# Optimization experiments

Hardware: AMD Instinct MI355X
Metric: run time of the kernel (lower is better)

The kernel has to match this reference:

```python
import jax, jax.numpy as jnp
import numpy as np

B, T, C = 2, 2048, 1024
H, D = 16, 64


def setup_inputs() -> dict:
    key = jax.random.key(0)
    k1, k2, k3 = jax.random.split(key, 3)
    x = jax.random.normal(k1, (B, T, C), dtype=jnp.float32)
    w_qkv = jax.random.normal(k2, (C, 3 * H * D), dtype=jnp.float32) * (C ** -0.5)
    w_proj = jax.random.normal(k3, (H * D, C), dtype=jnp.float32) * ((H * D) ** -0.5)
    sink_logit = jnp.zeros((H,), dtype=jnp.float32)
    return {"x": x, "w_qkv": w_qkv, "w_proj": w_proj, "sink_logit": sink_logit}


def reference(x, w_qkv, w_proj, sink_logit):
    b, t, c = x.shape
    qkv = x @ w_qkv                                  # [B,T,3HD]
    q, k, v = jnp.split(qkv, 3, axis=-1)
    # [B,H,T,D]
    q = q.reshape(b, t, H, D).transpose(0, 2, 1, 3)
    k = k.reshape(b, t, H, D).transpose(0, 2, 1, 3)
    v = v.reshape(b, t, H, D).transpose(0, 2, 1, 3)

    scale = 1.0 / jnp.sqrt(jnp.asarray(D, dtype=x.dtype))
    scores = jnp.einsum('bhqd,bhkd->bhqk', q, k) * scale   # [B,H,T,T]
    neg_inf = jnp.finfo(x.dtype).min
    causal = jnp.tril(jnp.ones((t, t), dtype=bool))
    scores = jnp.where(causal[None, None], scores, neg_inf)

    # sink column: per-head learnable logit b (added post-scale, V is zero)
    sink = jnp.broadcast_to(sink_logit.reshape(1, H, 1, 1), (b, H, t, 1)).astype(x.dtype)
    aug = jnp.concatenate([sink, scores], axis=-1)          # [B,H,T,T+1]
    attn = jax.nn.softmax(aug, axis=-1)
    # sink V is zero, so drop the sink column for the value contraction
    y = jnp.einsum('bhqk,bhkd->bhqd', attn[..., 1:], v)     # [B,H,T,D]
    y = y.transpose(0, 2, 1, 3).reshape(b, t, H * D)
    return y @ w_proj
```

## Files before the change

### kernel.cpp

```cpp
#include <hip/hip_runtime.h>
#include <hip/hip_bf16.h>
#include <stdint.h>

#define B_ 2
#define T_ 2048
#define C_ 1024
#define H_ 16
#define D_ 64

typedef __attribute__((ext_vector_type(8))) short short8;
typedef __attribute__((ext_vector_type(4))) float floatx4;

__device__ __forceinline__ float bf2f(uint16_t b) {
    return __uint_as_float(((uint32_t)b) << 16);
}
__device__ __forceinline__ uint16_t f2b(float f) {
    __hip_bfloat16 h = __float2bfloat16(f);
    return *(uint16_t*)&h;
}
__device__ __forceinline__ void glds16(const uint16_t* g, uint16_t* l) {
    __builtin_amdgcn_global_load_lds(
        (const __attribute__((address_space(1))) uint32_t*)g,
        (__attribute__((address_space(3))) uint32_t*)l, 16, 0, 0);
}

__global__ void canon_x(const float* __restrict__ in, uint16_t* __restrict__ out,
                        int n) {
    int i = (blockIdx.x * 256 + threadIdx.x) * 4;
    if (i >= n) return;
    float4 v = *(const float4*)(in + i);
    out[i + 0] = f2b(v.x);
    out[i + 1] = f2b(v.y);
    out[i + 2] = f2b(v.z);
    out[i + 3] = f2b(v.w);
}

__global__ void transpose_conv(const float* __restrict__ in, uint16_t* __restrict__ out,
                               int R, int W) {
    __shared__ uint16_t tile[32][33];
    int tx = threadIdx.x, ty = threadIdx.y;
    int c0 = blockIdx.x * 32, r0 = blockIdx.y * 32;
    #pragma unroll
    for (int i = 0; i < 32; i += 8)
        tile[ty + i][tx] = f2b(in[(size_t)(r0 + ty + i) * W + (c0 + tx)]);
    __syncthreads();
    #pragma unroll
    for (int i = 0; i < 32; i += 8)
        out[(size_t)(c0 + ty + i) * R + (r0 + tx)] = tile[tx][ty + i];
}

template <bool OUT_F32>
__global__ __launch_bounds__(256, 3)
void gemm_bt(const uint16_t* __restrict__ A, const uint16_t* __restrict__ Bt,
             void* __restrict__ Cv, int M, int N, int K) {
    __shared__ uint16_t As[3][128][32];
    __shared__ uint16_t Bs[3][128][32];
    int tid = threadIdx.x;
    int w = tid >> 6, lane = tid & 63;
    int quad = lane >> 4, l16 = lane & 15;
    int wr = (w >> 1) * 64, wc = (w & 1) * 64;

    int nwg = gridDim.x;
    int wg = (blockIdx.x & 7) * (nwg >> 3) + (blockIdx.x >> 3);
    int nby = N >> 7;
    int row0 = (wg / nby) * 128;
    int col0 = (wg % nby) * 128;

    int sr = w * 32 + (lane >> 2);
    int gsc = ((lane & 3) ^ ((lane >> 2) & 3)) * 8;
    uint16_t* lA0 = &As[0][sr][(lane & 3) * 8];
    uint16_t* lB0 = &Bs[0][sr][(lane & 3) * 8];
    const uint16_t* gA = A + (size_t)(row0 + sr) * K + gsc;
    const uint16_t* gB = Bt + (size_t)(col0 + sr) * K + gsc;

    floatx4 acc[4][4];
    #pragma unroll
    for (int i = 0; i < 4; i++)
        #pragma unroll
        for (int j = 0; j < 4; j++)
            acc[i][j] = (floatx4){0.f, 0.f, 0.f, 0.f};

#define STAGE3_(bs_, t_)                                                    \
    {                                                                       \
        const uint16_t* ga_ = gA + (size_t)(t_) * 32;                       \
        const uint16_t* gb_ = gB + (size_t)(t_) * 32;                       \
        uint16_t* la_ = lA0 + (bs_) * 4096;                                 \
        uint16_t* lb_ = lB0 + (bs_) * 4096;                                 \
        glds16(ga_, la_);                                                   \
        glds16(ga_ + 16 * K, la_ + 512);                                    \
        glds16(gb_, lb_);                                                   \
        glds16(gb_ + 16 * K, lb_ + 512);                                    \
    }

    int NT = K >> 5;
    STAGE3_(0, 0);
    STAGE3_(1, 1);
    asm volatile("s_waitcnt vmcnt(4)" ::: "memory");
    __builtin_amdgcn_s_barrier();

    const uint16_t* Ab = &As[0][0][0];
    const uint16_t* Bb = &Bs[0][0][0];
    int s = (quad ^ (l16 & 3)) * 8;
    int bc = 0, bs = 2;
    for (int t = 0; t < NT; ++t) {
        if (t + 2 < NT) STAGE3_(bs, t + 2);
        __builtin_amdgcn_sched_barrier(0);
        const uint16_t* Ac = Ab + bc * 4096;
        const uint16_t* Bc = Bb + bc * 4096;
        short8 af[4], bfr[4];
        #pragma unroll
        for (int i = 0; i < 4; i++)
            af[i] = *(const short8*)&Ac[(wr + i * 16 + l16) * 32 + s];
        #pragma unroll
        for (int j = 0; j < 4; j++)
            bfr[j] = *(const short8*)&Bc[(wc + j * 16 + l16) * 32 + s];
        #pragma unroll
        for (int i = 0; i < 4; i++)
            #pragma unroll
            for (int j = 0; j < 4; j++)
                acc[i][j] = __builtin_amdgcn_mfma_f32_16x16x32_bf16(
                    af[i], bfr[j], acc[i][j], 0, 0, 0);
        if (t + 2 < NT) {
            asm volatile("s_waitcnt vmcnt(4)" ::: "memory");
        } else {
            asm volatile("s_waitcnt vmcnt(0)" ::: "memory");
        }
        __builtin_amdgcn_s_barrier();
        bc = (bc == 2) ? 0 : bc + 1;
        bs = (bs == 2) ? 0 : bs + 1;
    }
#undef STAGE3_

    #pragma unroll
    for (int i = 0; i < 4; i++) {
        #pragma unroll
        for (int j = 0; j < 4; j++) {
            int rbase = row0 + wr + i * 16 + quad * 4;
            int cg = col0 + wc + j * 16 + l16;
            #pragma unroll
            for (int r = 0; r < 4; r++) {
                if (OUT_F32)
                    ((float*)Cv)[(size_t)(rbase + r) * N + cg] = acc[i][j][r];
                else
                    ((uint16_t*)Cv)[(size_t)(rbase + r) * N + cg] = f2b(acc[i][j][r]);
            }
        }
    }
}

__global__ __launch_bounds__(256, 2)
void attn_mfma(const uint16_t* __restrict__ qkv,
               const float* __restrict__ sink,
               uint16_t* __restrict__ y) {
    __shared__ uint16_t Ks[2][64][72];
    __shared__ uint16_t Vt[2][64][72];
    __shared__ uint16_t Pl[4][32][72];

    int tid = threadIdx.x;
    int w = tid >> 6, lane = tid & 63;
    int quad = lane >> 4, l16 = lane & 15;

    int id = blockIdx.x;
    int pair = id >> 5, bh = id & 31;
    int b = bh >> 4, h = bh & 15;
    int hi = 31 - pair, lo = pair;
    int q0s[2];
    q0s[0] = hi * 64 + w * 16;
    q0s[1] = lo * 64 + w * 16;
    int ktiles = hi + 1;
    int myk1 = lo + 1;

    const uint16_t* qkv_b = qkv + (size_t)b * T_ * 3072;

    short8 qf[2][2];
    #pragma unroll
    for (int qt = 0; qt < 2; qt++) {
        int qrow = q0s[qt] + l16;
        #pragma unroll
        for (int kd = 0; kd < 2; kd++) {
            uint4 raw = *(const uint4*)(qkv_b + (size_t)qrow * 3072 + h * 64 +
                                        kd * 32 + quad * 8);
            const uint16_t* rp = (const uint16_t*)&raw;
            short8 f;
            #pragma unroll
            for (int j = 0; j < 8; j++)
                f[j] = (short)f2b(bf2f(rp[j]) * 0.125f);
            qf[qt][kd] = f;
        }
    }

    float m_s[2], l_s[2];
    m_s[0] = m_s[1] = sink[h];
    l_s[0] = l_s[1] = 1.0f;
    floatx4 acc_o[2][4];
    #pragma unroll
    for (int qt = 0; qt < 2; qt++)
        #pragma unroll
        for (int dt = 0; dt < 4; dt++)
            acc_o[qt][dt] = (floatx4){0.f, 0.f, 0.f, 0.f};

    int t2 = tid >> 3;
    int dg = tid & 7;
    const uint16_t* kgp = qkv_b + 1024 + h * 64 + (size_t)(2 * t2) * 3072 + dg * 8;
    const uint16_t* vgp = kgp + 1024;
    int vcw = 2 * (t2 ^ (4 * dg));

    uint4 kr0 = *(const uint4*)(kgp);
    uint4 kr1 = *(const uint4*)(kgp + 3072);
    uint4 vr0 = *(const uint4*)(vgp);
    uint4 vr1 = *(const uint4*)(vgp + 3072);
    {
        *(uint4*)&Ks[0][2 * t2][dg * 8] = kr0;
        *(uint4*)&Ks[0][2 * t2 + 1][dg * 8] = kr1;
        const uint16_t* a0 = (const uint16_t*)&vr0;
        const uint16_t* a1 = (const uint16_t*)&vr1;
        #pragma unroll
        for (int j = 0; j < 8; j++)
            *(uint32_t*)&Vt[0][dg * 8 + j][vcw] =
                (uint32_t)a0[j] | ((uint32_t)a1[j] << 16);
    }
    if (ktiles > 1) {
        kr0 = *(const uint4*)(kgp + 64 * 3072);
        kr1 = *(const uint4*)(kgp + 64 * 3072 + 3072);
        vr0 = *(const uint4*)(vgp + 64 * 3072);
        vr1 = *(const uint4*)(vgp + 64 * 3072 + 3072);
    }
    __syncthreads();

    for (int kt = 0; kt < ktiles; kt++) {
        int cur = kt & 1;
        if (kt + 1 < ktiles) {
            *(uint4*)&Ks[cur ^ 1][2 * t2][dg * 8] = kr0;
            *(uint4*)&Ks[cur ^ 1][2 * t2 + 1][dg * 8] = kr1;
            const uint16_t* a0 = (const uint16_t*)&vr0;
            const uint16_t* a1 = (const uint16_t*)&vr1;
            #pragma unroll
            for (int j = 0; j < 8; j++)
                *(uint32_t*)&Vt[cur ^ 1][dg * 8 + j][vcw] =
                    (uint32_t)a0[j] | ((uint32_t)a1[j] << 16);
        }
        if (kt + 2 < ktiles) {
            size_t off = (size_t)(kt + 2) * 64 * 3072;
            kr0 = *(const uint4*)(kgp + off);
            kr1 = *(const uint4*)(kgp + off + 3072);
            vr0 = *(const uint4*)(vgp + off);
            vr1 = *(const uint4*)(vgp + off + 3072);
        }
        short8 kf[4][2];
        #pragma unroll
        for (int rt = 0; rt < 4; rt++) {
            kf[rt][0] = *(const short8*)&Ks[cur][rt * 16 + l16][quad * 8];
            kf[rt][1] = *(const short8*)&Ks[cur][rt * 16 + l16][32 + quad * 8];
        }
        short8 vf[2][4];
        #pragma unroll
        for (int kb = 0; kb < 2; kb++)
            #pragma unroll
            for (int dt = 0; dt < 4; dt++) {
                int d = dt * 16 + l16;
                int col = 2 * (((kb * 16) + quad * 4) ^ (4 * (d >> 3)));
                vf[kb][dt] = *(const short8*)&Vt[cur][d][col];
            }
        #pragma unroll
        for (int qt = 0; qt < 2; qt++) {
            if (qt == 1 && kt >= myk1) continue;
            floatx4 acc_s[4];
            #pragma unroll
            for (int rt = 0; rt < 4; rt++)
                acc_s[rt] = (floatx4){0.f, 0.f, 0.f, 0.f};
            #pragma unroll
            for (int rt = 0; rt < 4; rt++) {
                acc_s[rt] = __builtin_amdgcn_mfma_f32_16x16x32_bf16(
                    kf[rt][0], qf[qt][0], acc_s[rt], 0, 0, 0);
                acc_s[rt] = __builtin_amdgcn_mfma_f32_16x16x32_bf16(
                    kf[rt][1], qf[qt][1], acc_s[rt], 0, 0, 0);
            }
            int dqt = (qt == 0) ? hi : lo;
            if (kt == dqt) {
                int qg = q0s[qt] + l16;
                #pragma unroll
                for (int rt = 0; rt < 4; rt++) {
                    int kg = kt * 64 + rt * 16 + quad * 4;
                    #pragma unroll
                    for (int r = 0; r < 4; r++)
                        if (kg + r > qg) acc_s[rt][r] = -1e30f;
                }
            }
            float mx = -1e30f;
            #pragma unroll
            for (int rt = 0; rt < 4; rt++)
                #pragma unroll
                for (int r = 0; r < 4; r++) mx = fmaxf(mx, acc_s[rt][r]);
            mx = fmaxf(mx, __shfl_xor(mx, 16));
            mx = fmaxf(mx, __shfl_xor(mx, 32));
            float mnew = fmaxf(m_s[qt], mx);
            float alpha = __expf(m_s[qt] - mnew);
            m_s[qt] = mnew;
            float psum = 0.f;
            #pragma unroll
            for (int rt = 0; rt < 4; rt++) {
                float p0 = __expf(acc_s[rt][0] - mnew);
                float p1 = __expf(acc_s[rt][1] - mnew);
                float p2 = __expf(acc_s[rt][2] - mnew);
                float p3 = __expf(acc_s[rt][3] - mnew);
                psum += (p0 + p1) + (p2 + p3);
                uint2 pk;
                pk.x = (uint32_t)f2b(p0) | ((uint32_t)f2b(p1) << 16);
                pk.y = (uint32_t)f2b(p2) | ((uint32_t)f2b(p3) << 16);
                *(uint2*)&Pl[w][qt * 16 + l16][rt * 16 + quad * 4] = pk;
            }
            psum += __shfl_xor(psum, 16);
            psum += __shfl_xor(psum, 32);
            l_s[qt] = l_s[qt] * alpha + psum;
            #pragma unroll
            for (int r = 0; r < 4; r++) {
                float ar = __shfl(alpha, (lane & 48) | (quad * 4 + r));
                #pragma unroll
                for (int dt = 0; dt < 4; dt++) acc_o[qt][dt][r] *= ar;
            }
            #pragma unroll
            for (int kb = 0; kb < 2; kb++) {
                short8 pf = *(const short8*)&Pl[w][qt * 16 + l16][kb * 32 + quad * 8];
                #pragma unroll
                for (int dt = 0; dt < 4; dt++)
                    acc_o[qt][dt] = __builtin_amdgcn_mfma_f32_16x16x32_bf16(
                        pf, vf[kb][dt], acc_o[qt][dt], 0, 0, 0);
            }
        }
        __syncthreads();
    }

    #pragma unroll
    for (int qt = 0; qt < 2; qt++) {
        #pragma unroll
        for (int r = 0; r < 4; r++) {
            float lr = __shfl(l_s[qt], (lane & 48) | (quad * 4 + r));
            float inv = 1.0f / lr;
            int qg = q0s[qt] + quad * 4 + r;
            uint16_t* yp = y + (size_t)(b * T_ + qg) * 1024 + h * 64;
            #pragma unroll
            for (int dt = 0; dt < 4; dt++)
                yp[dt * 16 + l16] = f2b(acc_o[qt][dt][r] * inv);
        }
    }
}

extern "C" void kernel_launch(void* const* d_in, const int* in_sizes, int n_in,
                              void* d_out, int out_size, void* d_ws, size_t ws_size,
                              hipStream_t stream) {
    const float* x      = (const float*)d_in[0];
    const float* w_qkv  = (const float*)d_in[1];
    const float* w_proj = (const float*)d_in[2];
    const float* sink   = (const float*)d_in[3];
    float* out          = (float*)d_out;

    char* ws = (char*)d_ws;
    uint16_t* wt_qkv  = (uint16_t*)ws;
    uint16_t* wt_proj = (uint16_t*)(ws + 6291456);
    uint16_t* x_c     = (uint16_t*)(ws + 8388608);
    uint16_t* qkv     = (uint16_t*)(ws + 16777216);
    uint16_t* yb      = (uint16_t*)(ws + 41943040);

    canon_x<<<4194304 / 1024, 256, 0, stream>>>(x, x_c, 4194304);
    transpose_conv<<<dim3(3072 / 32, 1024 / 32), dim3(32, 8), 0, stream>>>(
        w_qkv, wt_qkv, 1024, 3072);
    transpose_conv<<<dim3(1024 / 32, 1024 / 32), dim3(32, 8), 0, stream>>>(
        w_proj, wt_proj, 1024, 1024);

    gemm_bt<false><<<dim3(768), 256, 0, stream>>>(
        x_c, wt_qkv, qkv, 4096, 3072, 1024);

    attn_mfma<<<dim3(16 * 32), 256, 0, stream>>>(qkv, sink, yb);

    gemm_bt<true><<<dim3(256), 256, 0, stream>>>(
        yb, wt_proj, out, 4096, 1024, 1024);
}
```

Baseline: 187.1 us.

## Fuse prep kernels, use exp2 softmax with lazy rescaling and packed bf16 convert

Merges the x-conversion and two weight-transpose kernels into a single prep launch to cut launch overhead. In attention, the log2(e) factor is folded into the Q scale and the sink logit so raw v_exp_f32 can replace __expf. The running max is only updated and the accumulators only rescaled when some lane's new max exceeds the old by more than 8, which skips the per-tile alpha shuffle and multiply in most iterations. P values are packed with v_cvt_pk_bf16_f32. The lazy threshold allows P values up to 2^8 before normalisation, which slightly changes numerics.

```diff
diff --git a/kernel.cpp b/kernel.cpp
--- a/kernel.cpp
+++ b/kernel.cpp
@@ -18,28 +18,51 @@
     __hip_bfloat16 h = __float2bfloat16(f);
     return *(uint16_t*)&h;
 }
+__device__ __forceinline__ float exp2v(float x) {
+    float r;
+    asm("v_exp_f32 %0, %1" : "=v"(r) : "v"(x));
+    return r;
+}
+__device__ __forceinline__ uint32_t cvtpk(float lo, float hi) {
+    uint32_t r;
+    asm("v_cvt_pk_bf16_f32 %0, %1, %2" : "=v"(r) : "v"(lo), "v"(hi));
+    return r;
+}
 __device__ __forceinline__ void glds16(const uint16_t* g, uint16_t* l) {
     __builtin_amdgcn_global_load_lds(
         (const __attribute__((address_space(1))) uint32_t*)g,
         (__attribute__((address_space(3))) uint32_t*)l, 16, 0, 0);
 }
 
-__global__ void canon_x(const float* __restrict__ in, uint16_t* __restrict__ out,
-                        int n) {
-    int i = (blockIdx.x * 256 + threadIdx.x) * 4;
-    if (i >= n) return;
-    float4 v = *(const float4*)(in + i);
-    out[i + 0] = f2b(v.x);
-    out[i + 1] = f2b(v.y);
-    out[i + 2] = f2b(v.z);
-    out[i + 3] = f2b(v.w);
-}
-
-__global__ void transpose_conv(const float* __restrict__ in, uint16_t* __restrict__ out,
-                               int R, int W) {
+__global__ void prep(const float* __restrict__ x, uint16_t* __restrict__ x_c,
+                     const float* __restrict__ w_qkv, uint16_t* __restrict__ wt_qkv,
+                     const float* __restrict__ w_proj, uint16_t* __restrict__ wt_proj) {
     __shared__ uint16_t tile[32][33];
-    int tx = threadIdx.x, ty = threadIdx.y;
-    int c0 = blockIdx.x * 32, r0 = blockIdx.y * 32;
+    int id = blockIdx.x;
+    int tid = threadIdx.x;
+    if (id < 4096) {
+        int i = (id * 256 + tid) * 4;
+        float4 v = *(const float4*)(x + i);
+        x_c[i + 0] = f2b(v.x);
+        x_c[i + 1] = f2b(v.y);
+        x_c[i + 2] = f2b(v.z);
+        x_c[i + 3] = f2b(v.w);
+        return;
+    }
+    const float* in;
+    uint16_t* out;
+    int R, W, bx, by;
+    if (id < 7168) {
+        int tb = id - 4096;
+        in = w_qkv; out = wt_qkv; R = 1024; W = 3072;
+        bx = tb % 96; by = tb / 96;
+    } else {
+        int tb = id - 7168;
+        in = w_proj; out = wt_proj; R = 1024; W = 1024;
+        bx = tb & 31; by = tb >> 5;
+    }
+    int tx = tid & 31, ty = tid >> 5;
+    int c0 = bx * 32, r0 = by * 32;
     #pragma unroll
     for (int i = 0; i < 32; i += 8)
         tile[ty + i][tx] = f2b(in[(size_t)(r0 + ty + i) * W + (c0 + tx)]);
@@ -172,6 +195,7 @@
 
     const uint16_t* qkv_b = qkv + (size_t)b * T_ * 3072;
 
+    const float QSC = 0.125f * 1.44269504f;
     short8 qf[2][2];
     #pragma unroll
     for (int qt = 0; qt < 2; qt++) {
@@ -184,13 +208,13 @@
             short8 f;
             #pragma unroll
             for (int j = 0; j < 8; j++)
-                f[j] = (short)f2b(bf2f(rp[j]) * 0.125f);
+                f[j] = (short)f2b(bf2f(rp[j]) * QSC);
             qf[qt][kd] = f;
         }
     }
 
     float m_s[2], l_s[2];
-    m_s[0] = m_s[1] = sink[h];
+    m_s[0] = m_s[1] = sink[h] * 1.44269504f;
     l_s[0] = l_s[1] = 1.0f;
     floatx4 acc_o[2][4];
     #pragma unroll
@@ -293,31 +317,36 @@
                 for (int r = 0; r < 4; r++) mx = fmaxf(mx, acc_s[rt][r]);
             mx = fmaxf(mx, __shfl_xor(mx, 16));
             mx = fmaxf(mx, __shfl_xor(mx, 32));
-            float mnew = fmaxf(m_s[qt], mx);
-            float alpha = __expf(m_s[qt] - mnew);
-            m_s[qt] = mnew;
+            float mold = m_s[qt];
+            if (!__all(mx <= mold + 8.0f)) {
+                float mnew = fmaxf(mold, mx);
+                float alpha = exp2v(mold - mnew);
+                m_s[qt] = mnew;
+                l_s[qt] *= alpha;
+                #pragma unroll
+                for (int r = 0; r < 4; r++) {
+                    float ar = __shfl(alpha, (lane & 48) | (quad * 4 + r));
+                    #pragma unroll
+                    for (int dt = 0; dt < 4; dt++) acc_o[qt][dt][r] *= ar;
+                }
+            }
+            float mcur = m_s[qt];
             float psum = 0.f;
             #pragma unroll
             for (int rt = 0; rt < 4; rt++) {
-                float p0 = __expf(acc_s[rt][0] - mnew);
-                float p1 = __expf(acc_s[rt][1] - mnew);
-                float p2 = __expf(acc_s[rt][2] - mnew);
-                float p3 = __expf(acc_s[rt][3] - mnew);
+                float p0 = exp2v(acc_s[rt][0] - mcur);
+                float p1 = exp2v(acc_s[rt][1] - mcur);
+                float p2 = exp2v(acc_s[rt][2] - mcur);
+                float p3 = exp2v(acc_s[rt][3] - mcur);
                 psum += (p0 + p1) + (p2 + p3);
                 uint2 pk;
-                pk.x = (uint32_t)f2b(p0) | ((uint32_t)f2b(p1) << 16);
-                pk.y = (uint32_t)f2b(p2) | ((uint32_t)f2b(p3) << 16);
+                pk.x = cvtpk(p0, p1);
+                pk.y = cvtpk(p2, p3);
                 *(uint2*)&Pl[w][qt * 16 + l16][rt * 16 + quad * 4] = pk;
             }
             psum += __shfl_xor(psum, 16);
             psum += __shfl_xor(psum, 32);
-            l_s[qt] = l_s[qt] * alpha + psum;
-            #pragma unroll
-            for (int r = 0; r < 4; r++) {
-                float ar = __shfl(alpha, (lane & 48) | (quad * 4 + r));
-                #pragma unroll
-                for (int dt = 0; dt < 4; dt++) acc_o[qt][dt][r] *= ar;
-            }
+            l_s[qt] += psum;
             #pragma unroll
             for (int kb = 0; kb < 2; kb++) {
                 short8 pf = *(const short8*)&Pl[w][qt * 16 + l16][kb * 32 + quad * 8];
@@ -361,11 +390,7 @@
     uint16_t* qkv     = (uint16_t*)(ws + 16777216);
     uint16_t* yb      = (uint16_t*)(ws + 41943040);
 
-    canon_x<<<4194304 / 1024, 256, 0, stream>>>(x, x_c, 4194304);
-    transpose_conv<<<dim3(3072 / 32, 1024 / 32), dim3(32, 8), 0, stream>>>(
-        w_qkv, wt_qkv, 1024, 3072);
-    transpose_conv<<<dim3(1024 / 32, 1024 / 32), dim3(32, 8), 0, stream>>>(
-        w_proj, wt_proj, 1024, 1024);
+    prep<<<dim3(8192), 256, 0, stream>>>(x, x_c, w_qkv, wt_qkv, w_proj, wt_proj);
 
     gemm_bt<false><<<dim3(768), 256, 0, stream>>>(
         x_c, wt_qkv, qkv, 4096, 3072, 1024);
```

Measured after the change: 181.1 us. 1.03x faster.
